# Performance work log

Measured on AMD Instinct MI355X. Metric: run time of the kernel, lower is better.

Reference implementation:

```python
import math
import jax, jax.numpy as jnp
import numpy as np
from jax import lax

B, C, H, W, D = 8, 3, 512, 512, 256
KS, SIGMA = 13, 2.0  # GaussianBlur(13); torchvision samples sigma in (0.1,5.0) -> fixed for determinism


def tanh01(v):
    return jnp.tanh(v) * 0.5 + 0.5


def tanh_range(v, left, right):
    return tanh01(v) * (right - left) + left


def norm01(v):
    return (v - v.min()) / (v.max() - v.min())


def gaussian_blur(x):
    r = KS // 2
    t = jnp.arange(KS, dtype=x.dtype) - r
    k = jnp.exp(-(t ** 2) / (2.0 * SIGMA ** 2))
    k = k / k.sum()
    b, c, h, w = x.shape
    xp = jnp.pad(x, ((0, 0), (0, 0), (r, r), (r, r)), mode='reflect').reshape(b * c, 1, h + 2 * r, w + 2 * r)
    y = lax.conv_general_dilated(xp, k.reshape(1, 1, KS, 1), (1, 1), 'VALID')
    y = lax.conv_general_dilated(y, k.reshape(1, 1, 1, KS), (1, 1), 'VALID')
    return y.reshape(b, c, h, w)


def dark_channel(x):
    return x.min(axis=1, keepdims=True)


def atmospheric_light(x, dark, top_k=1000):
    b, _, h, w = x.shape
    imsz = h * w
    numpx = max(imsz // top_k, 1)
    darkvec = dark.reshape(b, imsz)
    imvec = x.reshape(b, 3, imsz).transpose(0, 2, 1)  # [b, imsz, 3]
    idx = jnp.argsort(darkvec, axis=1)[:, imsz - numpx:]  # brightest dark-channel pixels
    gathered = jnp.take_along_axis(imvec, idx[:, :, None], axis=1)  # [b, numpx, 3]
    a = gathered[:, 1:, :].sum(axis=1) / numpx  # original loop skips index 0 of the slice
    return a[:, :, None, None]  # [b,3,1,1]


def fft_filter(x, rate, fft_gate):
    # rate: [b,1]; replicate torch.fft.fftshift default (shifts ALL axes, incl. batch/channel)
    b, c, w, h = x.shape  # note: original names w,h = shape[-2:]
    line = jnp.floor(jnp.sqrt(w * h * rate) / 2.0).astype(jnp.int32).reshape(-1)  # [b]
    rows = jnp.arange(w)
    cols = jnp.arange(h)
    mr = (rows[None, :] >= w // 2 - line[:, None]) & (rows[None, :] < w // 2 + line[:, None])
    mc = (cols[None, :] >= h // 2 - line[:, None]) & (cols[None, :] < h // 2 + line[:, None])
    mask = (mr[:, None, :, None] & mc[:, None, None, :]).astype(x.dtype)  # [b,1,w,h]
    mask = jnp.broadcast_to(mask, x.shape)
    F = jnp.fft.fftshift(jnp.fft.fft2(x, norm='forward'))
    F = F * (1.0 - mask)
    inv = jnp.fft.ifft2(jnp.fft.ifftshift(F), norm='forward').real
    return jnp.abs(inv) * fft_gate[:, None, None, None]


def setup_inputs() -> dict:
    key = jax.random.key(0)
    ks = jax.random.split(key, 20)
    def lin_w(k, i, o):
        return (jax.random.normal(k, (i, o)) * 0.02).astype(jnp.float32)
    def lin_b(k, o):
        return (jax.random.normal(k, (o,)) * 0.02).astype(jnp.float32)
    return {
        'x': jax.random.uniform(ks[0], (B, C, H, W), dtype=jnp.float32),
        'latent': (jax.random.normal(ks[1], (B, D)) * 0.5).astype(jnp.float32),
        'gate_w': lin_w(ks[2], D, 8), 'gate_b': lin_b(ks[3], 8),
        'wb_w': lin_w(ks[4], D, 3), 'wb_b': lin_b(ks[5], 3),
        'gamma_w': lin_w(ks[6], D, 1), 'gamma_b': lin_b(ks[7], 1),
        'sharp_w': lin_w(ks[8], D, 1), 'sharp_b': lin_b(ks[9], 1),
        'defog_w': lin_w(ks[10], D, 1), 'defog_b': lin_b(ks[11], 1),
        'contrast_w': lin_w(ks[12], D, 1), 'contrast_b': lin_b(ks[13], 1),
        'tone_w': lin_w(ks[14], D, 8), 'tone_b': lin_b(ks[15], 8),
        'fft_w': lin_w(ks[16], D, 1), 'fft_b': lin_b(ks[17], 1),
    }


def reference(x, latent, gate_w, gate_b, wb_w, wb_b, gamma_w, gamma_b, sharp_w, sharp_b,
              defog_w, defog_b, contrast_w, contrast_b, tone_w, tone_b, fft_w, fft_b):
    gate = tanh_range(latent @ gate_w + gate_b, 0.01, 1.0)  # [B,8]

    # white balance
    wb = jnp.exp(tanh_range(latent @ wb_w + wb_b, -0.5, 0.5))
    cs = 1.0 / (1e-5 + 0.27 * wb[:, 0] + 0.67 * wb[:, 1] + 0.06 * wb[:, 2])
    wb = cs[:, None] * wb
    wb_out = norm01(wb[:, :, None, None] * x) * gate[:, 0][:, None, None, None]

    # gamma balance
    lg = math.log(2.5)
    gamma = jnp.exp(tanh_range(latent @ gamma_w + gamma_b, -lg, lg))[:, :, None, None]
    g_out = norm01(jnp.maximum(x, 1e-4) ** gamma) * gate[:, 1][:, None, None, None]

    # identity
    id_out = x * gate[:, 2][:, None, None, None]

    # sharpening
    y = tanh_range(latent @ sharp_w + sharp_b, 0.1, 1.0)[:, :, None, None]
    s = x + y * (x - gaussian_blur(x))
    sharp_out = norm01(s) * gate[:, 3][:, None, None, None]

    # defog (atmospheric scattering model)
    omega = tanh_range(latent @ defog_w + defog_b, 0.1, 1.0)[:, :, None, None]
    dark = dark_channel(x)
    a = atmospheric_light(x, dark)
    t = 1.0 - omega * dark_channel(x / a)
    j = (x - a) / jnp.maximum(t, 0.01) + a
    fog_out = norm01(j) * gate[:, 4][:, None, None, None]

    # contrast
    alpha = jnp.tanh(latent @ contrast_w + contrast_b)[:, :, None, None]
    lum = jnp.clip(0.27 * x[:, 0] + 0.67 * x[:, 1] + 0.06 * x[:, 2], 0.0, 1.0)[:, None]
    clum = -jnp.cos(math.pi * lum) * 0.5 + 0.5
    cimg = x / (lum + 1e-6) * clum
    cimg = (1.0 - alpha) * x + alpha * cimg
    contrast_out = norm01(cimg) * gate[:, 5][:, None, None, None]

    # tone curve (8 fixed segments)
    tc = tanh_range(latent @ tone_w + tone_b, 0.5, 2.0)  # [B,8]
    tsum = tc.sum(axis=1) + 1e-30
    total = jnp.zeros_like(x)
    for i in range(8):
        total = total + jnp.clip(x - i / 8.0, 0.0, 1.0 / 8.0) * tc[:, i][:, None, None, None]
    total = total * (8.0 / tsum)[:, None, None, None]
    tone_out = norm01(total) * gate[:, 6][:, None, None, None]

    # fft frequency masking
    rate = tanh_range(latent @ fft_w + fft_b, 0.1, 0.8)  # [B,1]
    fft_out = fft_filter(x, rate, gate[:, 7])

    return norm01(wb_out + g_out + id_out + sharp_out + fog_out + contrast_out + tone_out + fft_out)
```

## Files before the change

### kernel.cpp

```cpp
#include <hip/hip_runtime.h>
#include <math.h>

#define HW 262144
#define TOTAL 6291456
#define PI_F 3.14159265358979323846f
#define NBIN 1024
#define PIDX(i) ((i) + ((i) >> 3))


#define PF_GATE 0
#define PF_WB 64
#define PF_GAMMA 88
#define PF_Y 96
#define PF_OMEGA 104
#define PF_ALPHA 112
#define PF_TC 120
#define PF_TSC 184
#define PF_RATE 192
#define PF_FG 200
#define PF_A 208
#define PF_WBM 256
#define PF_WBA 264
#define PF_GM 272
#define PF_GA 280
#define PF_SM 288
#define PF_SA 296
#define PF_FM 304
#define PF_FA 312
#define PF_CM 320
#define PF_CA 328
#define PF_TM 336
#define PF_TA 344
#define PF_LINE 360
#define PF_TCS 368
#define PF_TPRE 432
#define PF_IA 496

#define QX(b,c) ((b)*3+(c))
#define QS 24
#define QJ 25
#define QC 26
#define QFIN 27
#define SL_LCOUNT 1792
#define SL_BINSTAR 1920
#define SL_RNEED 1928
#define SL_SUMA2 2048

struct GK { float w[13]; };

__device__ __forceinline__ void waveFence(){ __builtin_amdgcn_wave_barrier(); }

__device__ __forceinline__ unsigned fkey(float f){
    unsigned u = __float_as_uint(f);
    return (u & 0x80000000u) ? ~u : (u | 0x80000000u);
}
__device__ __forceinline__ float funkey(unsigned k){
    return (k & 0x80000000u) ? __uint_as_float(k & 0x7FFFFFFFu) : __uint_as_float(~k);
}

__device__ __forceinline__ void blockRedPair(unsigned kmn, unsigned kmx, int q,
                                             unsigned* slots, unsigned* lds8){
    #pragma unroll
    for (int o = 32; o > 0; o >>= 1){
        kmn = min(kmn, __shfl_down(kmn, o));
        kmx = max(kmx, __shfl_down(kmx, o));
    }
    int w = threadIdx.x >> 6;
    if ((threadIdx.x & 63) == 0){ lds8[w] = kmn; lds8[4+w] = kmx; }
    __syncthreads();
    if (threadIdx.x == 0){
        unsigned mn = min(min(lds8[0],lds8[1]), min(lds8[2],lds8[3]));
        unsigned mx = max(max(lds8[4],lds8[5]), max(lds8[6],lds8[7]));
        int s = blockIdx.x & 31;
        atomicMin(&slots[q*64 + s], mn);
        atomicMax(&slots[q*64 + 32 + s], mx);
    }
    __syncthreads();
}

__device__ __forceinline__ float toneF(float v, const float* tc, float tsc){
    float tn = 0.f;
    #pragma unroll
    for (int i = 0; i < 8; ++i){
        float d = v - 0.125f * (float)i;
        d = fminf(fmaxf(d, 0.f), 0.125f);
        tn += d * tc[i];
    }
    return tn * tsc;
}

__device__ __forceinline__ float2 cadd(float2 a, float2 b){ return make_float2(a.x+b.x, a.y+b.y); }
__device__ __forceinline__ float2 csub(float2 a, float2 b){ return make_float2(a.x-b.x, a.y-b.y); }
__device__ __forceinline__ float2 cmul(float2 a, float2 b){ return make_float2(a.x*b.x - a.y*b.y, a.x*b.y + a.y*b.x); }

template<int S>
__device__ __forceinline__ float2 rot90(float2 z){
    return (S < 0) ? make_float2(z.y, -z.x) : make_float2(-z.y, z.x);
}

template<int S>
__device__ __forceinline__ void fft4p(float2 a, float2 b, float2 c, float2 d,
                                      float2& X0, float2& X1, float2& X2, float2& X3){
    float2 t0 = cadd(a,c), t1 = csub(a,c), t2 = cadd(b,d), t3 = csub(b,d);
    float2 it3 = rot90<S>(t3);
    X0 = cadd(t0,t2); X2 = csub(t0,t2);
    X1 = cadd(t1,it3); X3 = csub(t1,it3);
}

template<int S>
__device__ __forceinline__ void bfly8(float2 v[8]){
    const float C = 0.70710678118654752f;
    float2 E0,E1,E2,E3,O0,O1,O2,O3;
    fft4p<S>(v[0],v[2],v[4],v[6], E0,E1,E2,E3);
    fft4p<S>(v[1],v[3],v[5],v[7], O0,O1,O2,O3);
    float2 w1 = make_float2(C, (S<0) ? -C : C);
    float2 w3 = make_float2(-C, (S<0) ? -C : C);
    float2 u1 = cmul(O1, w1);
    float2 u2 = rot90<S>(O2);
    float2 u3 = cmul(O3, w3);
    v[0]=cadd(E0,O0); v[4]=csub(E0,O0);
    v[1]=cadd(E1,u1); v[5]=csub(E1,u1);
    v[2]=cadd(E2,u2); v[6]=csub(E2,u2);
    v[3]=cadd(E3,u3); v[7]=csub(E3,u3);
}

__device__ __forceinline__ void twiddles(float2 v[8], float th){
    float sn, cs; __sincosf(th, &sn, &cs);
    float2 w1 = make_float2(cs, sn);
    float2 w = w1;
    v[1] = cmul(v[1], w1);
    #pragma unroll
    for (int r = 2; r < 8; ++r){ w = cmul(w, w1); v[r] = cmul(v[r], w); }
}

template<int S>
__device__ __forceinline__ void fft512reg(float2 v[8], float2* buf, int lane){
    bfly8<S>(v);
    #pragma unroll
    for (int q = 0; q < 8; ++q) buf[PIDX(8*lane + q)] = v[q];
    waveFence();
    #pragma unroll
    for (int r = 0; r < 8; ++r) v[r] = buf[PIDX(lane + 64*r)];
    waveFence();
    twiddles(v, (float)S * 6.2831853072f * (float)(lane & 7) * (1.0f/64.0f));
    bfly8<S>(v);
    {
        int basei = ((lane >> 3) << 6) + (lane & 7);
        #pragma unroll
        for (int q = 0; q < 8; ++q) buf[PIDX(basei + 8*q)] = v[q];
    }
    waveFence();
    #pragma unroll
    for (int r = 0; r < 8; ++r) v[r] = buf[PIDX(lane + 64*r)];
    waveFence();
    twiddles(v, (float)S * 6.2831853072f * (float)lane * (1.0f/512.0f));
    bfly8<S>(v);
}

__global__ __launch_bounds__(256) void kSetup(
    const float* __restrict__ lat,
    const float* gw, const float* gb, const float* wbw, const float* wbb,
    const float* gaw, const float* gab, const float* shw, const float* shb,
    const float* dfw, const float* dfb, const float* ctw, const float* ctb,
    const float* tow, const float* tob, const float* ffw, const float* ffb,
    float* P, unsigned* slots, unsigned* hist)
{
    if (blockIdx.x != 0){
        int i = (blockIdx.x - 1) * 256 + threadIdx.x;
        if (i < 4096) slots[i] = (i < 1792 && (i & 63) < 32) ? 0xFFFFFFFFu : 0u;
        if (i < 8192) hist[i] = 0u;
        return;
    }
    int t = threadIdx.x;
    if (t < 192){
        int b = t / 24, o = t % 24;
        const float* L = lat + b * 256;
        const float* W; float bias; int nc, col;
        if (o < 8)      { W=gw;  bias=gb[o];     nc=8; col=o;    }
        else if (o < 11){ W=wbw; bias=wbb[o-8];  nc=3; col=o-8;  }
        else if (o==11) { W=gaw; bias=gab[0];    nc=1; col=0;    }
        else if (o==12) { W=shw; bias=shb[0];    nc=1; col=0;    }
        else if (o==13) { W=dfw; bias=dfb[0];    nc=1; col=0;    }
        else if (o==14) { W=ctw; bias=ctb[0];    nc=1; col=0;    }
        else if (o<23)  { W=tow; bias=tob[o-15]; nc=8; col=o-15; }
        else            { W=ffw; bias=ffb[0];    nc=1; col=0;    }
        float acc = bias;
        for (int d = 0; d < 256; ++d) acc += L[d] * W[d*nc + col];
        float t01 = tanhf(acc) * 0.5f + 0.5f;
        if (o < 8){ float v = t01*0.99f + 0.01f; P[PF_GATE + b*8 + o] = v; if (o==7) P[PF_FG + b] = v; }
        else if (o < 11){ P[PF_WB + b*3 + (o-8)] = expf(t01 - 0.5f); }
        else if (o==11){ float lg = logf(2.5f); P[PF_GAMMA + b] = expf(t01*(2.f*lg) - lg); }
        else if (o==12){ P[PF_Y + b] = t01*0.9f + 0.1f; }
        else if (o==13){ P[PF_OMEGA + b] = t01*0.9f + 0.1f; }
        else if (o==14){ P[PF_ALPHA + b] = tanhf(acc); }
        else if (o<23){ P[PF_TC + b*8 + (o-15)] = t01*1.5f + 0.5f; }
        else { P[PF_RATE + b] = t01*0.7f + 0.1f; }
    }
    __syncthreads();
    if (t < 8){
        int b = t;
        float w0=P[PF_WB+b*3], w1=P[PF_WB+b*3+1], w2=P[PF_WB+b*3+2];
        float cs = 1.0f / (1e-5f + 0.27f*w0 + 0.67f*w1 + 0.06f*w2);
        P[PF_WB+b*3] = cs*w0; P[PF_WB+b*3+1] = cs*w1; P[PF_WB+b*3+2] = cs*w2;
        float ts = 0.f;
        for (int i = 0; i < 8; ++i) ts += P[PF_TC + b*8 + i];
        float tsc = 8.0f / (ts + 1e-30f);
        P[PF_TSC + b] = tsc;
        float acc = 0.f;
        for (int k = 0; k < 8; ++k){
            float tck = P[PF_TC + b*8 + k] * tsc;
            P[PF_TCS + b*8 + k] = tck;
            P[PF_TPRE + b*8 + k] = acc;
            acc += tck * 0.125f;
        }
        int bs = (b + 4) & 7;
        ((int*)(P + PF_LINE))[b] = (int)floorf(sqrtf(262144.0f * P[PF_RATE + bs]) * 0.5f);
    }
}

__global__ __launch_bounds__(256) void kMinmaxHist(const float* __restrict__ x, unsigned* slots, unsigned* hist){
    __shared__ unsigned h[NBIN];
    __shared__ unsigned lds8[8];
    int b = blockIdx.x >> 7;
    int blk = blockIdx.x & 127;
    for (int i = threadIdx.x; i < NBIN; i += 256) h[i] = 0u;
    __syncthreads();
    size_t xb = (size_t)b*3*HW;
    int p0 = (((blk<<1)    )*256 + threadIdx.x) << 2;
    int p1 = (((blk<<1) + 1)*256 + threadIdx.x) << 2;
    float4 u0 = *(const float4*)(x + xb + p0);
    float4 u1 = *(const float4*)(x + xb + HW + p0);
    float4 u2 = *(const float4*)(x + xb + 2*HW + p0);
    float4 w0 = *(const float4*)(x + xb + p1);
    float4 w1 = *(const float4*)(x + xb + HW + p1);
    float4 w2 = *(const float4*)(x + xb + 2*HW + p1);
    float a0[8] = {u0.x,u0.y,u0.z,u0.w, w0.x,w0.y,w0.z,w0.w};
    float a1[8] = {u1.x,u1.y,u1.z,u1.w, w1.x,w1.y,w1.z,w1.w};
    float a2[8] = {u2.x,u2.y,u2.z,u2.w, w2.x,w2.y,w2.z,w2.w};
    float mn0=1e30f,mx0=-1e30f,mn1=1e30f,mx1=-1e30f,mn2=1e30f,mx2=-1e30f;
    #pragma unroll
    for (int e = 0; e < 8; ++e){
        float dark = fminf(a0[e], fminf(a1[e], a2[e]));
        atomicAdd(&h[min(NBIN-1, (int)(dark * (float)NBIN))], 1u);
        mn0 = fminf(mn0, a0[e]); mx0 = fmaxf(mx0, a0[e]);
        mn1 = fminf(mn1, a1[e]); mx1 = fmaxf(mx1, a1[e]);
        mn2 = fminf(mn2, a2[e]); mx2 = fmaxf(mx2, a2[e]);
    }
    __syncthreads();
    for (int i = threadIdx.x; i < NBIN; i += 256){
        unsigned c = h[i];
        if (c) atomicAdd(&hist[b*NBIN + i], c);
    }
    blockRedPair(fkey(mn0), fkey(mx0), QX(b,0), slots, lds8);
    blockRedPair(fkey(mn1), fkey(mx1), QX(b,1), slots, lds8);
    blockRedPair(fkey(mn2), fkey(mx2), QX(b,2), slots, lds8);
}

__global__ __launch_bounds__(256) void kScanHist(const unsigned* __restrict__ hist, unsigned* slots){
    int b = blockIdx.x, t = threadIdx.x;
    __shared__ unsigned wtot[4];
    __shared__ int doneS;
    if (t == 0) doneS = 0;
    __syncthreads();
    unsigned total = 0;
    for (int c0 = 0; c0 < NBIN; c0 += 256){
        int binIdx = NBIN-1 - (c0 + t);
        unsigned cnt = hist[b*NBIN + binIdx];
        unsigned v = cnt;
        #pragma unroll
        for (int off = 1; off < 64; off <<= 1){
            unsigned u = __shfl_up(v, off);
            if ((t & 63) >= off) v += u;
        }
        if ((t & 63) == 63) wtot[t >> 6] = v;
        __syncthreads();
        unsigned wofs = 0;
        for (int w = 0; w < (t >> 6); ++w) wofs += wtot[w];
        unsigned incl = total + wofs + v;
        unsigned excl = incl - cnt;
        if (incl >= 261u && excl < 261u){
            slots[SL_BINSTAR + b] = (unsigned)binIdx;
            slots[SL_RNEED + b]   = 261u - excl;
            doneS = 1;
        }
        __syncthreads();
        if (doneS) break;
        total += wtot[0] + wtot[1] + wtot[2] + wtot[3];
        __syncthreads();
    }
}

__global__ __launch_bounds__(256) void kCollect(const float* __restrict__ x, unsigned* slots, uint2* list){
    __shared__ float wsum[3][4];
    int b = blockIdx.x >> 8;
    int tile = blockIdx.x & 255;
    size_t xb = (size_t)b*3*HW;
    int p = (tile*256 + threadIdx.x) << 2;
    float4 v0 = *(const float4*)(x + xb + p);
    float4 v1 = *(const float4*)(x + xb + HW + p);
    float4 v2 = *(const float4*)(x + xb + 2*HW + p);
    int bs = (int)slots[SL_BINSTAR + b];
    float a0[4] = {v0.x,v0.y,v0.z,v0.w};
    float a1[4] = {v1.x,v1.y,v1.z,v1.w};
    float a2[4] = {v2.x,v2.y,v2.z,v2.w};
    float s0 = 0.f, s1 = 0.f, s2 = 0.f;
    #pragma unroll
    for (int e = 0; e < 4; ++e){
        float dark = fminf(a0[e], fminf(a1[e], a2[e]));
        int bin = min(NBIN-1, (int)(dark * (float)NBIN));
        if (bin > bs){ s0 += a0[e]; s1 += a1[e]; s2 += a2[e]; }
        else if (bin == bs){
            unsigned n = atomicAdd(&slots[SL_LCOUNT + b], 1u);
            if (n < 1024u) list[(b << 10) + n] = make_uint2(__float_as_uint(dark), (unsigned)(p + e));
        }
    }
    #pragma unroll
    for (int o = 32; o > 0; o >>= 1){
        s0 += __shfl_down(s0, o); s1 += __shfl_down(s1, o); s2 += __shfl_down(s2, o);
    }
    int w = threadIdx.x >> 6;
    if ((threadIdx.x & 63) == 0){ wsum[0][w] = s0; wsum[1][w] = s1; wsum[2][w] = s2; }
    __syncthreads();
    if (threadIdx.x == 0){
        float t0 = wsum[0][0]+wsum[0][1]+wsum[0][2]+wsum[0][3];
        float t1 = wsum[1][0]+wsum[1][1]+wsum[1][2]+wsum[1][3];
        float t2 = wsum[2][0]+wsum[2][1]+wsum[2][2]+wsum[2][3];
        float* F = (float*)(slots + SL_SUMA2);
        int sl = blockIdx.x & 31;
        atomicAdd(&F[(b*3+0)*32 + sl], t0);
        atomicAdd(&F[(b*3+1)*32 + sl], t1);
        atomicAdd(&F[(b*3+2)*32 + sl], t2);
    }
}

__global__ void kSelect(const float* __restrict__ x, uint2* list, unsigned* slots, float* P){
    __shared__ unsigned pid[262];
    __shared__ char taken[1024];
    int b = blockIdx.x, t = threadIdx.x;
    int n = (int)min(slots[SL_LCOUNT + b], 1024u);
    int r = (int)slots[SL_RNEED + b];
    if (r > n) r = n;
    const uint2* L = &list[b << 10];
    for (int i = t; i < n; i += 64) taken[i] = 0;
    __syncthreads();
    for (int it = 0; it < r; ++it){
        unsigned long long bk = 0ull; int bp = -1;
        for (int i = t; i < n; i += 64){
            if (taken[i]) continue;
            uint2 e = L[i];
            unsigned long long key = ((unsigned long long)e.x << 32) | e.y;
            if (key > bk){ bk = key; bp = i; }
        }
        #pragma unroll
        for (int o = 32; o > 0; o >>= 1){
            unsigned long long ok = __shfl_down(bk, o);
            int op = __shfl_down(bp, o);
            if (ok > bk){ bk = ok; bp = op; }
        }
        bp = __shfl(bp, 0);
        if (t == 0){ pid[it] = L[bp].y; taken[bp] = 1; }
        __syncthreads();
    }
    float s0 = 0.f, s1 = 0.f, s2 = 0.f;
    size_t xb = (size_t)b*3*HW;
    for (int i = t; i < r; i += 64){
        unsigned id = pid[i];
        s0 += x[xb + id]; s1 += x[xb + HW + id]; s2 += x[xb + 2*HW + id];
    }
    #pragma unroll
    for (int o = 32; o > 0; o >>= 1){
        s0 += __shfl_down(s0, o); s1 += __shfl_down(s1, o); s2 += __shfl_down(s2, o);
    }
    if (t == 0){
        const float* F = (const float*)(slots + SL_SUMA2);
        float f0 = 0.f, f1 = 0.f, f2 = 0.f;
        for (int k = 0; k < 32; ++k){
            f0 += F[(b*3+0)*32 + k];
            f1 += F[(b*3+1)*32 + k];
            f2 += F[(b*3+2)*32 + k];
        }
        float A0 = (s0 + f0) / 262.0f, A1 = (s1 + f1) / 262.0f, A2 = (s2 + f2) / 262.0f;
        P[PF_A + b*3+0] = A0; P[PF_A + b*3+1] = A1; P[PF_A + b*3+2] = A2;
        P[PF_IA + b*3+0] = 1.0f/A0; P[PF_IA + b*3+1] = 1.0f/A1; P[PF_IA + b*3+2] = 1.0f/A2;
    }
}

__global__ __launch_bounds__(256) void kBlur(const float* __restrict__ x, float* __restrict__ sharpOut,
                                             const float* __restrict__ P, unsigned* slots, GK gk){
    __shared__ float tile[76][80];
    __shared__ float hbuf[76][68];
    __shared__ unsigned lds8[8];
    int img = blockIdx.x >> 6;
    int tid = blockIdx.x & 63;
    int tr0 = (tid >> 3) << 6;
    int tc0 = (tid & 7) << 6;
    size_t ib = (size_t)img * HW;
    int t = threadIdx.x;
    for (int l = t; l < 76*76; l += 256){
        int r = l / 76, c = l - r*76;
        int gr = tr0 + r - 6; gr = (gr < 0) ? -gr : ((gr > 511) ? 1022 - gr : gr);
        int gc = tc0 + c - 6; gc = (gc < 0) ? -gc : ((gc > 511) ? 1022 - gc : gc);
        tile[r][c] = x[ib + ((size_t)gr << 9) + gc];
    }
    __syncthreads();
    for (int l = t; l < 76*64; l += 256){
        int r = l >> 6, c = l & 63;
        float acc = 0.f;
        #pragma unroll
        for (int k = 0; k < 13; ++k) acc += gk.w[k] * tile[r][c + k];
        hbuf[r][c] = acc;
    }
    __syncthreads();
    float yb = P[PF_Y + img/3];
    unsigned kmn = 0xFFFFFFFFu, kmx = 0u;
    for (int l = t; l < 64*64; l += 256){
        int r = l >> 6, c = l & 63;
        float acc = 0.f;
        #pragma unroll
        for (int k = 0; k < 13; ++k) acc += gk.w[k] * hbuf[r + k][c];
        float xv = tile[r + 6][c + 6];
        float s = xv + yb * (xv - acc);
        sharpOut[ib + ((size_t)(tr0 + r) << 9) + tc0 + c] = s;
        unsigned key = fkey(s);
        kmn = min(kmn, key); kmx = max(kmx, key);
    }
    blockRedPair(kmn, kmx, QS, slots, lds8);
}

__global__ __launch_bounds__(256) void kFftRowFwdJC(const float* __restrict__ x, float2* __restrict__ bc,
                                                    const float* __restrict__ P, unsigned* slots){
    __shared__ float2 buf4[4][580];
    __shared__ unsigned lds8[8];
    float (*xs)[3][512] = reinterpret_cast<float(*)[3][512]>(&buf4[0][0]);
    int b = blockIdx.x >> 8;
    int rp = blockIdx.x & 255;
    int t = threadIdx.x;
    #pragma unroll
    for (int k = 0; k < 3; ++k){
        int l = t + (k << 8);
        int seg = l >> 7;
        int idx = (l & 127) << 2;
        int ch = seg >> 1, rr = seg & 1;
        float4 z = *(const float4*)(x + (size_t)(3*b + ch)*HW + ((size_t)(2*rp + rr) << 9) + idx);
        *(float4*)&xs[rr][ch][idx] = z;
    }
    __syncthreads();
    {
        float ia0 = P[PF_IA+b*3], ia1 = P[PF_IA+b*3+1], ia2 = P[PF_IA+b*3+2];
        float a0 = P[PF_A+b*3],  a1 = P[PF_A+b*3+1],  a2 = P[PF_A+b*3+2];
        float om = P[PF_OMEGA+b], al = P[PF_ALPHA+b];
        int rr = t >> 7, c4 = (t & 127) << 2;
        float4 xv0 = *(float4*)&xs[rr][0][c4];
        float4 xv1 = *(float4*)&xs[rr][1][c4];
        float4 xv2 = *(float4*)&xs[rr][2][c4];
        float A0[4]={xv0.x,xv0.y,xv0.z,xv0.w}, A1[4]={xv1.x,xv1.y,xv1.z,xv1.w}, A2[4]={xv2.x,xv2.y,xv2.z,xv2.w};
        float jmn = 1e30f, jmx = -1e30f, cmn = 1e30f, cmx = -1e30f;
        #pragma unroll
        for (int e = 0; e < 4; ++e){
            float x0 = A0[e], x1 = A1[e], x2 = A2[e];
            float dr = fminf(x0*ia0, fminf(x1*ia1, x2*ia2));
            float T = fmaxf(1.0f - om*dr, 0.01f);
            float rT = 1.0f / T;
            float j0 = (x0-a0)*rT + a0, j1 = (x1-a1)*rT + a1, j2 = (x2-a2)*rT + a2;
            float lum = fminf(fmaxf(0.27f*x0 + 0.67f*x1 + 0.06f*x2, 0.f), 1.f);
            float clum = -__cosf(PI_F*lum)*0.5f + 0.5f;
            float alx = (1.f - al) + al * (clum / (lum + 1e-6f));
            float c0 = x0*alx, c1 = x1*alx, c2 = x2*alx;
            jmn = fminf(jmn, fminf(j0, fminf(j1, j2))); jmx = fmaxf(jmx, fmaxf(j0, fmaxf(j1, j2)));
            cmn = fminf(cmn, fminf(c0, fminf(c1, c2))); cmx = fmaxf(cmx, fmaxf(c0, fmaxf(c1, c2)));
        }
        blockRedPair(fkey(jmn), fkey(jmx), QJ, slots, lds8);
        blockRedPair(fkey(cmn), fkey(cmx), QC, slots, lds8);
    }
    int u = t >> 6, lane = t & 63;
    int frr = u >> 1, pk = u & 1;
    float2 v[8];
    #pragma unroll
    for (int r = 0; r < 8; ++r){
        int i = lane + 64*r;
        if (pk == 0) v[r] = make_float2(xs[frr][0][i] * (1.0f/512.0f), xs[frr][1][i] * (1.0f/512.0f));
        else         v[r] = make_float2(xs[frr][2][i] * (1.0f/512.0f), 0.f);
    }
    __syncthreads();
    fft512reg<-1>(v, buf4[u], lane);
    size_t ob = (size_t)(2*b + pk)*HW + ((size_t)(2*rp + frr) << 9);
    #pragma unroll
    for (int q = 0; q < 8; ++q) bc[ob + lane + 64*q] = v[q];
}

__global__ __launch_bounds__(256) void kFftColMid(float2* __restrict__ bc, const int* __restrict__ lineS){
    int img  = blockIdx.x >> 6;
    int tile = blockIdx.x & 63;
    int c0 = tile << 3;
    int line = lineS[img >> 1];
    if (c0 >= line && c0 + 8 <= 512 - line) return;
    __shared__ float2 cb[8][580];
    int t = threadIdx.x;
    size_t ibase = (size_t)img*HW + c0;
    for (int k = 0; k < 16; ++k){
        int idx = (k << 8) + t;
        int row = idx >> 3, col = idx & 7;
        float2 z = bc[ibase + ((size_t)row << 9) + col];
        cb[col][PIDX(row)] = make_float2(z.x * (1.0f/512.0f), z.y * (1.0f/512.0f));
    }
    __syncthreads();
    int lane = t & 63, u = t >> 6;
    #pragma unroll
    for (int h = 0; h < 2; ++h){
        int col = (h << 2) + u;
        int cc = c0 + col;
        bool colM = (cc < line) || (cc >= 512 - line);
        float2 v[8];
        #pragma unroll
        for (int r = 0; r < 8; ++r) v[r] = cb[col][PIDX(lane + 64*r)];
        waveFence();
        fft512reg<-1>(v, cb[col], lane);
        if (colM){
            #pragma unroll
            for (int q = 0; q < 8; ++q){
                int f = lane + (q << 6);
                if (f < line || f >= 512 - line) v[q] = make_float2(0.f, 0.f);
            }
        }
        waveFence();
        fft512reg<+1>(v, cb[col], lane);
        #pragma unroll
        for (int q = 0; q < 8; ++q) cb[col][PIDX(lane + 64*q)] = v[q];
        waveFence();
    }
    __syncthreads();
    for (int k = 0; k < 16; ++k){
        int idx = (k << 8) + t;
        int row = idx >> 3, col = idx & 7;
        int cc = c0 + col;
        if (cc < line || cc >= 512 - line)
            bc[ibase + ((size_t)row << 9) + col] = cb[col][PIDX(row)];
    }
}

__global__ __launch_bounds__(256) void kCombineFFT(const float* __restrict__ x, float* __restrict__ outb,
                                                   const float2* __restrict__ bc, const float* __restrict__ P,
                                                   unsigned* slots){
    __shared__ float2 buf4[4][580];
    __shared__ float stc[8], spre[8];
    __shared__ unsigned lds8[8];
    float (*fbuf)[3][512] = reinterpret_cast<float(*)[3][512]>(&buf4[0][0]);
    int b = blockIdx.x >> 8;
    int rp = blockIdx.x & 255;
    int t = threadIdx.x;
    if (t < 8){ stc[t] = P[PF_TCS + b*8 + t]; spre[t] = P[PF_TPRE + b*8 + t]; }
    int u = t >> 6, lane = t & 63;
    int frr = u >> 1, pk = u & 1;
    float2 v[8];
    size_t ib = (size_t)(2*b + pk)*HW + ((size_t)(2*rp + frr) << 9);
    #pragma unroll
    for (int r = 0; r < 8; ++r) v[r] = bc[ib + lane + 64*r];
    fft512reg<+1>(v, buf4[u], lane);
    __syncthreads();
    if (pk == 0){
        #pragma unroll
        for (int q = 0; q < 8; ++q){
            int i = lane + 64*q;
            fbuf[frr][0][i] = fabsf(v[q].x);
            fbuf[frr][1][i] = fabsf(v[q].y);
        }
    } else {
        #pragma unroll
        for (int q = 0; q < 8; ++q) fbuf[frr][2][lane + 64*q] = fabsf(v[q].x);
    }
    __syncthreads();

    float g  = P[PF_FG + b];
    float wb0=P[PF_WB+b*3], wb1=P[PF_WB+b*3+1], wb2=P[PF_WB+b*3+2];
    float gam=P[PF_GAMMA+b], om=P[PF_OMEGA+b], al=P[PF_ALPHA+b];
    float a0=P[PF_A+b*3], a1=P[PF_A+b*3+1], a2=P[PF_A+b*3+2];
    float ia0=P[PF_IA+b*3], ia1=P[PF_IA+b*3+1], ia2=P[PF_IA+b*3+2];
    float g2=P[PF_GATE+b*8+2];
    float wbm=P[PF_WBM+b], wba=P[PF_WBA+b], gm=P[PF_GM+b], ga=P[PF_GA+b];
    float sm=P[PF_SM+b], sa=P[PF_SA+b], fm=P[PF_FM+b], fa=P[PF_FA+b];
    float cm=P[PF_CM+b], ca=P[PF_CA+b], tm=P[PF_TM+b], ta=P[PF_TA+b];
    float kadd = wba + ga + sa + fa + ca + ta;
    float cw0 = wb0*wbm + g2, cw1 = wb1*wbm + g2, cw2 = wb2*wbm + g2;

    int rr = t >> 7, c4 = (t & 127) << 2;
    size_t p0 = (size_t)(3*b)*HW + ((size_t)(2*rp + rr) << 9) + c4;
    float4 xv0 = *(const float4*)(x + p0);
    float4 xv1 = *(const float4*)(x + p0 + HW);
    float4 xv2 = *(const float4*)(x + p0 + 2*HW);
    float4 sv0 = *(const float4*)(outb + p0);
    float4 sv1 = *(const float4*)(outb + p0 + HW);
    float4 sv2 = *(const float4*)(outb + p0 + 2*HW);
    float4 fv0 = *(float4*)&fbuf[rr][0][c4];
    float4 fv1 = *(float4*)&fbuf[rr][1][c4];
    float4 fv2 = *(float4*)&fbuf[rr][2][c4];
    float X0[4]={xv0.x,xv0.y,xv0.z,xv0.w}, X1[4]={xv1.x,xv1.y,xv1.z,xv1.w}, X2[4]={xv2.x,xv2.y,xv2.z,xv2.w};
    float S0[4]={sv0.x,sv0.y,sv0.z,sv0.w}, S1[4]={sv1.x,sv1.y,sv1.z,sv1.w}, S2[4]={sv2.x,sv2.y,sv2.z,sv2.w};
    float F0[4]={fv0.x,fv0.y,fv0.z,fv0.w}, F1[4]={fv1.x,fv1.y,fv1.z,fv1.w}, F2[4]={fv2.x,fv2.y,fv2.z,fv2.w};
    float O0[4], O1[4], O2[4];
    float mn = 1e30f, mx = -1e30f;
    #pragma unroll
    for (int e = 0; e < 4; ++e){
        float x0 = X0[e], x1 = X1[e], x2 = X2[e];
        float dr = fminf(x0*ia0, fminf(x1*ia1, x2*ia2));
        float T = fmaxf(1.0f - om*dr, 0.01f);
        float rT = 1.0f / T;
        float lum = fminf(fmaxf(0.27f*x0 + 0.67f*x1 + 0.06f*x2, 0.f), 1.f);
        float clum = -__cosf(PI_F*lum)*0.5f + 0.5f;
        float alx = (1.f - al) + al * (clum / (lum + 1e-6f));
        {
            float j = (x0 - a0)*rT + a0;
            int k = min(7, (int)(x0 * 8.0f));
            float tn = spre[k] + (x0 - 0.125f*(float)k) * stc[k];
            float gp = __powf(fmaxf(x0, 1e-4f), gam);
            float sum = x0*cw0 + gp*gm + S0[e]*sm + j*fm + (x0*alx)*cm + tn*tm + kadd + F0[e]*g;
            O0[e] = sum; mn = fminf(mn, sum); mx = fmaxf(mx, sum);
        }
        {
            float j = (x1 - a1)*rT + a1;
            int k = min(7, (int)(x1 * 8.0f));
            float tn = spre[k] + (x1 - 0.125f*(float)k) * stc[k];
            float gp = __powf(fmaxf(x1, 1e-4f), gam);
            float sum = x1*cw1 + gp*gm + S1[e]*sm + j*fm + (x1*alx)*cm + tn*tm + kadd + F1[e]*g;
            O1[e] = sum; mn = fminf(mn, sum); mx = fmaxf(mx, sum);
        }
        {
            float j = (x2 - a2)*rT + a2;
            int k = min(7, (int)(x2 * 8.0f));
            float tn = spre[k] + (x2 - 0.125f*(float)k) * stc[k];
            float gp = __powf(fmaxf(x2, 1e-4f), gam);
            float sum = x2*cw2 + gp*gm + S2[e]*sm + j*fm + (x2*alx)*cm + tn*tm + kadd + F2[e]*g;
            O2[e] = sum; mn = fminf(mn, sum); mx = fmaxf(mx, sum);
        }
    }
    *(float4*)(outb + p0)        = make_float4(O0[0],O0[1],O0[2],O0[3]);
    *(float4*)(outb + p0 + HW)   = make_float4(O1[0],O1[1],O1[2],O1[3]);
    *(float4*)(outb + p0 + 2*HW) = make_float4(O2[0],O2[1],O2[2],O2[3]);
    blockRedPair(fkey(mn), fkey(mx), QFIN, slots, lds8);
}

__global__ void kNormParams(float* P, const unsigned* __restrict__ slots){
    __shared__ float mnv[28], mxv[28];
    int t = threadIdx.x;
    if (t < 28){
        unsigned kmn = 0xFFFFFFFFu, kmx = 0u;
        for (int s = 0; s < 32; ++s){
            kmn = min(kmn, slots[t*64 + s]);
            kmx = max(kmx, slots[t*64 + 32 + s]);
        }
        mnv[t] = funkey(kmn); mxv[t] = funkey(kmx);
    }
    __syncthreads();
    if (t == 0){
        float wmin=1e30f, wmax=-1e30f, gmin=1e30f, gmax=-1e30f, tmin=1e30f, tmax=-1e30f;
        for (int b = 0; b < 8; ++b){
            float gam = P[PF_GAMMA+b];
            float tsc = P[PF_TSC+b];
            const float* tc = &P[PF_TC + b*8];
            float xbmin = 1e30f, xbmax = -1e30f;
            for (int c = 0; c < 3; ++c){
                int i = b*3 + c;
                float w = P[PF_WB + i];
                wmin = fminf(wmin, w * mnv[i]); wmax = fmaxf(wmax, w * mxv[i]);
                gmin = fminf(gmin, __powf(fmaxf(mnv[i], 1e-4f), gam));
                gmax = fmaxf(gmax, __powf(fmaxf(mxv[i], 1e-4f), gam));
                xbmin = fminf(xbmin, mnv[i]); xbmax = fmaxf(xbmax, mxv[i]);
            }
            tmin = fminf(tmin, toneF(xbmin, tc, tsc));
            tmax = fmaxf(tmax, toneF(xbmax, tc, tsc));
        }
        float smin = mnv[QS], smax = mxv[QS];
        float jmin = mnv[QJ], jmax = mxv[QJ];
        float cmin = mnv[QC], cmax = mxv[QC];
        for (int b = 0; b < 8; ++b){
            const float* G = &P[PF_GATE + b*8];
            float m;
            m = G[0]/(wmax-wmin); P[PF_WBM+b]=m; P[PF_WBA+b]=-wmin*m;
            m = G[1]/(gmax-gmin); P[PF_GM +b]=m; P[PF_GA +b]=-gmin*m;
            m = G[3]/(smax-smin); P[PF_SM +b]=m; P[PF_SA +b]=-smin*m;
            m = G[4]/(jmax-jmin); P[PF_FM +b]=m; P[PF_FA +b]=-jmin*m;
            m = G[5]/(cmax-cmin); P[PF_CM +b]=m; P[PF_CA +b]=-cmin*m;
            m = G[6]/(tmax-tmin); P[PF_TM +b]=m; P[PF_TA +b]=-tmin*m;
        }
    }
}

__global__ __launch_bounds__(256) void kFinalNorm(float* __restrict__ out, const unsigned* __restrict__ slots){
    unsigned kmn = 0xFFFFFFFFu, kmx = 0u;
    for (int s = 0; s < 32; ++s){
        kmn = min(kmn, slots[QFIN*64 + s]);
        kmx = max(kmx, slots[QFIN*64 + 32 + s]);
    }
    float mn = funkey(kmn), mx = funkey(kmx);
    float inv = 1.0f / (mx - mn);
    size_t i = ((size_t)blockIdx.x*256 + threadIdx.x) << 2;
    float4 v = *(const float4*)(out + i);
    v.x = (v.x - mn) * inv; v.y = (v.y - mn) * inv;
    v.z = (v.z - mn) * inv; v.w = (v.w - mn) * inv;
    *(float4*)(out + i) = v;
}

extern "C" void kernel_launch(void* const* d_in, const int* in_sizes, int n_in,
                              void* d_out, int out_size, void* d_ws, size_t ws_size,
                              hipStream_t stream){
    const float* x   = (const float*)d_in[0];
    const float* lat = (const float*)d_in[1];
    const float* gw  = (const float*)d_in[2];  const float* gb  = (const float*)d_in[3];
    const float* wbw = (const float*)d_in[4];  const float* wbb = (const float*)d_in[5];
    const float* gaw = (const float*)d_in[6];  const float* gab = (const float*)d_in[7];
    const float* shw = (const float*)d_in[8];  const float* shb = (const float*)d_in[9];
    const float* dfw = (const float*)d_in[10]; const float* dfb = (const float*)d_in[11];
    const float* ctw = (const float*)d_in[12]; const float* ctb = (const float*)d_in[13];
    const float* tow = (const float*)d_in[14]; const float* tob = (const float*)d_in[15];
    const float* ffw = (const float*)d_in[16]; const float* ffb = (const float*)d_in[17];
    float* out = (float*)d_out;
    char* ws = (char*)d_ws;

    float*    P     = (float*)ws;
    unsigned* slots = (unsigned*)(ws + 4096);
    unsigned* hist  = (unsigned*)(ws + 20480);
    uint2*    list  = (uint2*)(ws + 540672);
    float2*   bufC  = (float2*)(ws + 1048576);
    const int* lineS = (const int*)(P + PF_LINE);

    GK gk;
    {
        float s = 0.f;
        for (int i = 0; i < 13; ++i){ float t = (float)i - 6.f; gk.w[i] = expf(-(t*t)/8.0f); s += gk.w[i]; }
        for (int i = 0; i < 13; ++i) gk.w[i] /= s;
    }

    hipLaunchKernelGGL(kSetup,       dim3(41),   dim3(256), 0, stream, lat, gw,gb,wbw,wbb,gaw,gab,shw,shb,dfw,dfb,ctw,ctb,tow,tob,ffw,ffb, P, slots, hist);
    hipLaunchKernelGGL(kMinmaxHist,  dim3(1024), dim3(256), 0, stream, x, slots, hist);
    hipLaunchKernelGGL(kScanHist,    dim3(8),    dim3(256), 0, stream, hist, slots);
    hipLaunchKernelGGL(kCollect,     dim3(2048), dim3(256), 0, stream, x, slots, list);
    hipLaunchKernelGGL(kSelect,      dim3(8),    dim3(64),  0, stream, x, list, slots, P);
    hipLaunchKernelGGL(kBlur,        dim3(1536), dim3(256), 0, stream, x, out, P, slots, gk);
    hipLaunchKernelGGL(kFftRowFwdJC, dim3(2048), dim3(256), 0, stream, x, bufC, P, slots);
    hipLaunchKernelGGL(kFftColMid,   dim3(1024), dim3(256), 0, stream, bufC, lineS);
    hipLaunchKernelGGL(kNormParams,  dim3(1),    dim3(64),  0, stream, P, slots);
    hipLaunchKernelGGL(kCombineFFT,  dim3(2048), dim3(256), 0, stream, x, out, bufC, P, slots);
    hipLaunchKernelGGL(kFinalNorm,   dim3(6144), dim3(256), 0, stream, out, slots);
}
```

Measured before the change: 200.4 us.

## Merge independent stages into combined launches to overlap FFT, histogram and blur work

```diff
diff --git a/kernel.cpp b/kernel.cpp
--- a/kernel.cpp
+++ b/kernel.cpp
@@ -218,42 +218,76 @@
     }
 }
 
-__global__ __launch_bounds__(256) void kMinmaxHist(const float* __restrict__ x, unsigned* slots, unsigned* hist){
-    __shared__ unsigned h[NBIN];
+__global__ __launch_bounds__(256) void kHistRowFwd(const float* __restrict__ x, float2* __restrict__ bc,
+                                                   unsigned* slots, unsigned* hist){
+    __shared__ float2 buf4[4][580];
     __shared__ unsigned lds8[8];
-    int b = blockIdx.x >> 7;
-    int blk = blockIdx.x & 127;
-    for (int i = threadIdx.x; i < NBIN; i += 256) h[i] = 0u;
-    __syncthreads();
-    size_t xb = (size_t)b*3*HW;
-    int p0 = (((blk<<1)    )*256 + threadIdx.x) << 2;
-    int p1 = (((blk<<1) + 1)*256 + threadIdx.x) << 2;
-    float4 u0 = *(const float4*)(x + xb + p0);
-    float4 u1 = *(const float4*)(x + xb + HW + p0);
-    float4 u2 = *(const float4*)(x + xb + 2*HW + p0);
-    float4 w0 = *(const float4*)(x + xb + p1);
-    float4 w1 = *(const float4*)(x + xb + HW + p1);
-    float4 w2 = *(const float4*)(x + xb + 2*HW + p1);
-    float a0[8] = {u0.x,u0.y,u0.z,u0.w, w0.x,w0.y,w0.z,w0.w};
-    float a1[8] = {u1.x,u1.y,u1.z,u1.w, w1.x,w1.y,w1.z,w1.w};
-    float a2[8] = {u2.x,u2.y,u2.z,u2.w, w2.x,w2.y,w2.z,w2.w};
-    float mn0=1e30f,mx0=-1e30f,mn1=1e30f,mx1=-1e30f,mn2=1e30f,mx2=-1e30f;
-    #pragma unroll
-    for (int e = 0; e < 8; ++e){
-        float dark = fminf(a0[e], fminf(a1[e], a2[e]));
-        atomicAdd(&h[min(NBIN-1, (int)(dark * (float)NBIN))], 1u);
-        mn0 = fminf(mn0, a0[e]); mx0 = fmaxf(mx0, a0[e]);
-        mn1 = fminf(mn1, a1[e]); mx1 = fmaxf(mx1, a1[e]);
-        mn2 = fminf(mn2, a2[e]); mx2 = fmaxf(mx2, a2[e]);
-    }
-    __syncthreads();
-    for (int i = threadIdx.x; i < NBIN; i += 256){
-        unsigned c = h[i];
-        if (c) atomicAdd(&hist[b*NBIN + i], c);
-    }
-    blockRedPair(fkey(mn0), fkey(mx0), QX(b,0), slots, lds8);
-    blockRedPair(fkey(mn1), fkey(mx1), QX(b,1), slots, lds8);
-    blockRedPair(fkey(mn2), fkey(mx2), QX(b,2), slots, lds8);
+    int t = threadIdx.x;
+    if (blockIdx.x < 2048){
+        float (*xs)[3][512] = reinterpret_cast<float(*)[3][512]>(&buf4[0][0]);
+        int b = blockIdx.x >> 8;
+        int rp = blockIdx.x & 255;
+        #pragma unroll
+        for (int k = 0; k < 3; ++k){
+            int l = t + (k << 8);
+            int seg = l >> 7;
+            int idx = (l & 127) << 2;
+            int ch = seg >> 1, rr = seg & 1;
+            float4 z = *(const float4*)(x + (size_t)(3*b + ch)*HW + ((size_t)(2*rp + rr) << 9) + idx);
+            *(float4*)&xs[rr][ch][idx] = z;
+        }
+        __syncthreads();
+        int u = t >> 6, lane = t & 63;
+        int frr = u >> 1, pk = u & 1;
+        float2 v[8];
+        #pragma unroll
+        for (int r = 0; r < 8; ++r){
+            int i = lane + 64*r;
+            if (pk == 0) v[r] = make_float2(xs[frr][0][i] * (1.0f/512.0f), xs[frr][1][i] * (1.0f/512.0f));
+            else         v[r] = make_float2(xs[frr][2][i] * (1.0f/512.0f), 0.f);
+        }
+        __syncthreads();
+        fft512reg<-1>(v, buf4[u], lane);
+        size_t ob = (size_t)(2*b + pk)*HW + ((size_t)(2*rp + frr) << 9);
+        #pragma unroll
+        for (int q = 0; q < 8; ++q) bc[ob + lane + 64*q] = v[q];
+    } else {
+        unsigned* h = (unsigned*)&buf4[0][0];
+        int hb = blockIdx.x - 2048;
+        int b = hb >> 7;
+        int blk = hb & 127;
+        for (int i = t; i < NBIN; i += 256) h[i] = 0u;
+        __syncthreads();
+        size_t xb = (size_t)b*3*HW;
+        int p0 = (((blk<<1)    )*256 + t) << 2;
+        int p1 = (((blk<<1) + 1)*256 + t) << 2;
+        float4 u0 = *(const float4*)(x + xb + p0);
+        float4 u1 = *(const float4*)(x + xb + HW + p0);
+        float4 u2 = *(const float4*)(x + xb + 2*HW + p0);
+        float4 w0 = *(const float4*)(x + xb + p1);
+        float4 w1 = *(const float4*)(x + xb + HW + p1);
+        float4 w2 = *(const float4*)(x + xb + 2*HW + p1);
+        float a0[8] = {u0.x,u0.y,u0.z,u0.w, w0.x,w0.y,w0.z,w0.w};
+        float a1[8] = {u1.x,u1.y,u1.z,u1.w, w1.x,w1.y,w1.z,w1.w};
+        float a2[8] = {u2.x,u2.y,u2.z,u2.w, w2.x,w2.y,w2.z,w2.w};
+        float mn0=1e30f,mx0=-1e30f,mn1=1e30f,mx1=-1e30f,mn2=1e30f,mx2=-1e30f;
+        #pragma unroll
+        for (int e = 0; e < 8; ++e){
+            float dark = fminf(a0[e], fminf(a1[e], a2[e]));
+            atomicAdd(&h[min(NBIN-1, (int)(dark * (float)NBIN))], 1u);
+            mn0 = fminf(mn0, a0[e]); mx0 = fmaxf(mx0, a0[e]);
+            mn1 = fminf(mn1, a1[e]); mx1 = fmaxf(mx1, a1[e]);
+            mn2 = fminf(mn2, a2[e]); mx2 = fmaxf(mx2, a2[e]);
+        }
+        __syncthreads();
+        for (int i = t; i < NBIN; i += 256){
+            unsigned c = h[i];
+            if (c) atomicAdd(&hist[b*NBIN + i], c);
+        }
+        blockRedPair(fkey(mn0), fkey(mx0), QX(b,0), slots, lds8);
+        blockRedPair(fkey(mn1), fkey(mx1), QX(b,1), slots, lds8);
+        blockRedPair(fkey(mn2), fkey(mx2), QX(b,2), slots, lds8);
+    }
 }
 
 __global__ __launch_bounds__(256) void kScanHist(const unsigned* __restrict__ hist, unsigned* slots){
@@ -290,46 +324,139 @@
     }
 }
 
-__global__ __launch_bounds__(256) void kCollect(const float* __restrict__ x, unsigned* slots, uint2* list){
-    __shared__ float wsum[3][4];
-    int b = blockIdx.x >> 8;
-    int tile = blockIdx.x & 255;
-    size_t xb = (size_t)b*3*HW;
-    int p = (tile*256 + threadIdx.x) << 2;
-    float4 v0 = *(const float4*)(x + xb + p);
-    float4 v1 = *(const float4*)(x + xb + HW + p);
-    float4 v2 = *(const float4*)(x + xb + 2*HW + p);
-    int bs = (int)slots[SL_BINSTAR + b];
-    float a0[4] = {v0.x,v0.y,v0.z,v0.w};
-    float a1[4] = {v1.x,v1.y,v1.z,v1.w};
-    float a2[4] = {v2.x,v2.y,v2.z,v2.w};
-    float s0 = 0.f, s1 = 0.f, s2 = 0.f;
-    #pragma unroll
-    for (int e = 0; e < 4; ++e){
-        float dark = fminf(a0[e], fminf(a1[e], a2[e]));
-        int bin = min(NBIN-1, (int)(dark * (float)NBIN));
-        if (bin > bs){ s0 += a0[e]; s1 += a1[e]; s2 += a2[e]; }
-        else if (bin == bs){
-            unsigned n = atomicAdd(&slots[SL_LCOUNT + b], 1u);
-            if (n < 1024u) list[(b << 10) + n] = make_uint2(__float_as_uint(dark), (unsigned)(p + e));
-        }
-    }
-    #pragma unroll
-    for (int o = 32; o > 0; o >>= 1){
-        s0 += __shfl_down(s0, o); s1 += __shfl_down(s1, o); s2 += __shfl_down(s2, o);
-    }
-    int w = threadIdx.x >> 6;
-    if ((threadIdx.x & 63) == 0){ wsum[0][w] = s0; wsum[1][w] = s1; wsum[2][w] = s2; }
-    __syncthreads();
-    if (threadIdx.x == 0){
-        float t0 = wsum[0][0]+wsum[0][1]+wsum[0][2]+wsum[0][3];
-        float t1 = wsum[1][0]+wsum[1][1]+wsum[1][2]+wsum[1][3];
-        float t2 = wsum[2][0]+wsum[2][1]+wsum[2][2]+wsum[2][3];
-        float* F = (float*)(slots + SL_SUMA2);
-        int sl = blockIdx.x & 31;
-        atomicAdd(&F[(b*3+0)*32 + sl], t0);
-        atomicAdd(&F[(b*3+1)*32 + sl], t1);
-        atomicAdd(&F[(b*3+2)*32 + sl], t2);
+__global__ __launch_bounds__(256) void kCCB(const float* __restrict__ x, float2* __restrict__ bc,
+                                            const int* __restrict__ lineS, unsigned* slots, uint2* list,
+                                            const float* __restrict__ P, float* __restrict__ sharpOut, GK gk){
+    __shared__ __align__(16) char smem[45056];
+    int t = threadIdx.x;
+    if (blockIdx.x < 1024){
+        int img  = blockIdx.x >> 6;
+        int tile = blockIdx.x & 63;
+        int c0 = tile << 3;
+        int line = lineS[img >> 1];
+        if (c0 >= line && c0 + 8 <= 512 - line) return;
+        float2 (*cb)[580] = reinterpret_cast<float2(*)[580]>(smem);
+        size_t ibase = (size_t)img*HW + c0;
+        for (int k = 0; k < 16; ++k){
+            int idx = (k << 8) + t;
+            int row = idx >> 3, col = idx & 7;
+            float2 z = bc[ibase + ((size_t)row << 9) + col];
+            cb[col][PIDX(row)] = make_float2(z.x * (1.0f/512.0f), z.y * (1.0f/512.0f));
+        }
+        __syncthreads();
+        int lane = t & 63, u = t >> 6;
+        #pragma unroll
+        for (int h = 0; h < 2; ++h){
+            int col = (h << 2) + u;
+            int cc = c0 + col;
+            bool colM = (cc < line) || (cc >= 512 - line);
+            float2 v[8];
+            #pragma unroll
+            for (int r = 0; r < 8; ++r) v[r] = cb[col][PIDX(lane + 64*r)];
+            waveFence();
+            fft512reg<-1>(v, cb[col], lane);
+            if (colM){
+                #pragma unroll
+                for (int q = 0; q < 8; ++q){
+                    int f = lane + (q << 6);
+                    if (f < line || f >= 512 - line) v[q] = make_float2(0.f, 0.f);
+                }
+            }
+            waveFence();
+            fft512reg<+1>(v, cb[col], lane);
+            #pragma unroll
+            for (int q = 0; q < 8; ++q) cb[col][PIDX(lane + 64*q)] = v[q];
+            waveFence();
+        }
+        __syncthreads();
+        for (int k = 0; k < 16; ++k){
+            int idx = (k << 8) + t;
+            int row = idx >> 3, col = idx & 7;
+            int cc = c0 + col;
+            if (cc < line || cc >= 512 - line)
+                bc[ibase + ((size_t)row << 9) + col] = cb[col][PIDX(row)];
+        }
+    } else if (blockIdx.x < 3072){
+        float (*wsum)[4] = reinterpret_cast<float(*)[4]>(smem);
+        int cbk = blockIdx.x - 1024;
+        int b = cbk >> 8;
+        int tile = cbk & 255;
+        size_t xb = (size_t)b*3*HW;
+        int p = (tile*256 + t) << 2;
+        float4 v0 = *(const float4*)(x + xb + p);
+        float4 v1 = *(const float4*)(x + xb + HW + p);
+        float4 v2 = *(const float4*)(x + xb + 2*HW + p);
+        int bs = (int)slots[SL_BINSTAR + b];
+        float a0[4] = {v0.x,v0.y,v0.z,v0.w};
+        float a1[4] = {v1.x,v1.y,v1.z,v1.w};
+        float a2[4] = {v2.x,v2.y,v2.z,v2.w};
+        float s0 = 0.f, s1 = 0.f, s2 = 0.f;
+        #pragma unroll
+        for (int e = 0; e < 4; ++e){
+            float dark = fminf(a0[e], fminf(a1[e], a2[e]));
+            int bin = min(NBIN-1, (int)(dark * (float)NBIN));
+            if (bin > bs){ s0 += a0[e]; s1 += a1[e]; s2 += a2[e]; }
+            else if (bin == bs){
+                unsigned n = atomicAdd(&slots[SL_LCOUNT + b], 1u);
+                if (n < 1024u) list[(b << 10) + n] = make_uint2(__float_as_uint(dark), (unsigned)(p + e));
+            }
+        }
+        #pragma unroll
+        for (int o = 32; o > 0; o >>= 1){
+            s0 += __shfl_down(s0, o); s1 += __shfl_down(s1, o); s2 += __shfl_down(s2, o);
+        }
+        int w = t >> 6;
+        if ((t & 63) == 0){ wsum[0][w] = s0; wsum[1][w] = s1; wsum[2][w] = s2; }
+        __syncthreads();
+        if (t == 0){
+            float t0 = wsum[0][0]+wsum[0][1]+wsum[0][2]+wsum[0][3];
+            float t1 = wsum[1][0]+wsum[1][1]+wsum[1][2]+wsum[1][3];
+            float t2 = wsum[2][0]+wsum[2][1]+wsum[2][2]+wsum[2][3];
+            float* F = (float*)(slots + SL_SUMA2);
+            int sl = blockIdx.x & 31;
+            atomicAdd(&F[(b*3+0)*32 + sl], t0);
+            atomicAdd(&F[(b*3+1)*32 + sl], t1);
+            atomicAdd(&F[(b*3+2)*32 + sl], t2);
+        }
+    } else {
+        float (*tile)[80] = reinterpret_cast<float(*)[80]>(smem);
+        float (*hbuf)[68] = reinterpret_cast<float(*)[68]>(smem + 24320);
+        unsigned* lds8 = reinterpret_cast<unsigned*>(smem + 44992);
+        int bb = blockIdx.x - 3072;
+        int img = bb >> 6;
+        int tid = bb & 63;
+        int tr0 = (tid >> 3) << 6;
+        int tc0 = (tid & 7) << 6;
+        size_t ib = (size_t)img * HW;
+        for (int l = t; l < 76*76; l += 256){
+            int r = l / 76, c = l - r*76;
+            int gr = tr0 + r - 6; gr = (gr < 0) ? -gr : ((gr > 511) ? 1022 - gr : gr);
+            int gc = tc0 + c - 6; gc = (gc < 0) ? -gc : ((gc > 511) ? 1022 - gc : gc);
+            tile[r][c] = x[ib + ((size_t)gr << 9) + gc];
+        }
+        __syncthreads();
+        for (int l = t; l < 76*64; l += 256){
+            int r = l >> 6, c = l & 63;
+            float acc = 0.f;
+            #pragma unroll
+            for (int k = 0; k < 13; ++k) acc += gk.w[k] * tile[r][c + k];
+            hbuf[r][c] = acc;
+        }
+        __syncthreads();
+        float yb = P[PF_Y + img/3];
+        unsigned kmn = 0xFFFFFFFFu, kmx = 0u;
+        for (int l = t; l < 64*64; l += 256){
+            int r = l >> 6, c = l & 63;
+            float acc = 0.f;
+            #pragma unroll
+            for (int k = 0; k < 13; ++k) acc += gk.w[k] * hbuf[r + k][c];
+            float xv = tile[r + 6][c + 6];
+            float s = xv + yb * (xv - acc);
+            sharpOut[ib + ((size_t)(tr0 + r) << 9) + tc0 + c] = s;
+            unsigned key = fkey(s);
+            kmn = min(kmn, key); kmx = max(kmx, key);
+        }
+        blockRedPair(kmn, kmx, QS, slots, lds8);
     }
 }
 
@@ -385,257 +512,38 @@
     }
 }
 
-__global__ __launch_bounds__(256) void kBlur(const float* __restrict__ x, float* __restrict__ sharpOut,
-                                             const float* __restrict__ P, unsigned* slots, GK gk){
-    __shared__ float tile[76][80];
-    __shared__ float hbuf[76][68];
+__global__ __launch_bounds__(256) void kJCMinmax(const float* __restrict__ x, const float* __restrict__ P, unsigned* slots){
     __shared__ unsigned lds8[8];
-    int img = blockIdx.x >> 6;
-    int tid = blockIdx.x & 63;
-    int tr0 = (tid >> 3) << 6;
-    int tc0 = (tid & 7) << 6;
-    size_t ib = (size_t)img * HW;
-    int t = threadIdx.x;
-    for (int l = t; l < 76*76; l += 256){
-        int r = l / 76, c = l - r*76;
-        int gr = tr0 + r - 6; gr = (gr < 0) ? -gr : ((gr > 511) ? 1022 - gr : gr);
-        int gc = tc0 + c - 6; gc = (gc < 0) ? -gc : ((gc > 511) ? 1022 - gc : gc);
-        tile[r][c] = x[ib + ((size_t)gr << 9) + gc];
-    }
-    __syncthreads();
-    for (int l = t; l < 76*64; l += 256){
-        int r = l >> 6, c = l & 63;
-        float acc = 0.f;
-        #pragma unroll
-        for (int k = 0; k < 13; ++k) acc += gk.w[k] * tile[r][c + k];
-        hbuf[r][c] = acc;
-    }
-    __syncthreads();
-    float yb = P[PF_Y + img/3];
-    unsigned kmn = 0xFFFFFFFFu, kmx = 0u;
-    for (int l = t; l < 64*64; l += 256){
-        int r = l >> 6, c = l & 63;
-        float acc = 0.f;
-        #pragma unroll
-        for (int k = 0; k < 13; ++k) acc += gk.w[k] * hbuf[r + k][c];
-        float xv = tile[r + 6][c + 6];
-        float s = xv + yb * (xv - acc);
-        sharpOut[ib + ((size_t)(tr0 + r) << 9) + tc0 + c] = s;
-        unsigned key = fkey(s);
-        kmn = min(kmn, key); kmx = max(kmx, key);
-    }
-    blockRedPair(kmn, kmx, QS, slots, lds8);
-}
-
-__global__ __launch_bounds__(256) void kFftRowFwdJC(const float* __restrict__ x, float2* __restrict__ bc,
-                                                    const float* __restrict__ P, unsigned* slots){
-    __shared__ float2 buf4[4][580];
-    __shared__ unsigned lds8[8];
-    float (*xs)[3][512] = reinterpret_cast<float(*)[3][512]>(&buf4[0][0]);
     int b = blockIdx.x >> 8;
-    int rp = blockIdx.x & 255;
-    int t = threadIdx.x;
-    #pragma unroll
-    for (int k = 0; k < 3; ++k){
-        int l = t + (k << 8);
-        int seg = l >> 7;
-        int idx = (l & 127) << 2;
-        int ch = seg >> 1, rr = seg & 1;
-        float4 z = *(const float4*)(x + (size_t)(3*b + ch)*HW + ((size_t)(2*rp + rr) << 9) + idx);
-        *(float4*)&xs[rr][ch][idx] = z;
-    }
-    __syncthreads();
-    {
-        float ia0 = P[PF_IA+b*3], ia1 = P[PF_IA+b*3+1], ia2 = P[PF_IA+b*3+2];
-        float a0 = P[PF_A+b*3],  a1 = P[PF_A+b*3+1],  a2 = P[PF_A+b*3+2];
-        float om = P[PF_OMEGA+b], al = P[PF_ALPHA+b];
-        int rr = t >> 7, c4 = (t & 127) << 2;
-        float4 xv0 = *(float4*)&xs[rr][0][c4];
-        float4 xv1 = *(float4*)&xs[rr][1][c4];
-        float4 xv2 = *(float4*)&xs[rr][2][c4];
-        float A0[4]={xv0.x,xv0.y,xv0.z,xv0.w}, A1[4]={xv1.x,xv1.y,xv1.z,xv1.w}, A2[4]={xv2.x,xv2.y,xv2.z,xv2.w};
-        float jmn = 1e30f, jmx = -1e30f, cmn = 1e30f, cmx = -1e30f;
-        #pragma unroll
-        for (int e = 0; e < 4; ++e){
-            float x0 = A0[e], x1 = A1[e], x2 = A2[e];
-            float dr = fminf(x0*ia0, fminf(x1*ia1, x2*ia2));
-            float T = fmaxf(1.0f - om*dr, 0.01f);
-            float rT = 1.0f / T;
-            float j0 = (x0-a0)*rT + a0, j1 = (x1-a1)*rT + a1, j2 = (x2-a2)*rT + a2;
-            float lum = fminf(fmaxf(0.27f*x0 + 0.67f*x1 + 0.06f*x2, 0.f), 1.f);
-            float clum = -__cosf(PI_F*lum)*0.5f + 0.5f;
-            float alx = (1.f - al) + al * (clum / (lum + 1e-6f));
-            float c0 = x0*alx, c1 = x1*alx, c2 = x2*alx;
-            jmn = fminf(jmn, fminf(j0, fminf(j1, j2))); jmx = fmaxf(jmx, fmaxf(j0, fmaxf(j1, j2)));
-            cmn = fminf(cmn, fminf(c0, fminf(c1, c2))); cmx = fmaxf(cmx, fmaxf(c0, fmaxf(c1, c2)));
-        }
-        blockRedPair(fkey(jmn), fkey(jmx), QJ, slots, lds8);
-        blockRedPair(fkey(cmn), fkey(cmx), QC, slots, lds8);
-    }
-    int u = t >> 6, lane = t & 63;
-    int frr = u >> 1, pk = u & 1;
-    float2 v[8];
-    #pragma unroll
-    for (int r = 0; r < 8; ++r){
-        int i = lane + 64*r;
-        if (pk == 0) v[r] = make_float2(xs[frr][0][i] * (1.0f/512.0f), xs[frr][1][i] * (1.0f/512.0f));
-        else         v[r] = make_float2(xs[frr][2][i] * (1.0f/512.0f), 0.f);
-    }
-    __syncthreads();
-    fft512reg<-1>(v, buf4[u], lane);
-    size_t ob = (size_t)(2*b + pk)*HW + ((size_t)(2*rp + frr) << 9);
-    #pragma unroll
-    for (int q = 0; q < 8; ++q) bc[ob + lane + 64*q] = v[q];
-}
-
-__global__ __launch_bounds__(256) void kFftColMid(float2* __restrict__ bc, const int* __restrict__ lineS){
-    int img  = blockIdx.x >> 6;
-    int tile = blockIdx.x & 63;
-    int c0 = tile << 3;
-    int line = lineS[img >> 1];
-    if (c0 >= line && c0 + 8 <= 512 - line) return;
-    __shared__ float2 cb[8][580];
-    int t = threadIdx.x;
-    size_t ibase = (size_t)img*HW + c0;
-    for (int k = 0; k < 16; ++k){
-        int idx = (k << 8) + t;
-        int row = idx >> 3, col = idx & 7;
-        float2 z = bc[ibase + ((size_t)row << 9) + col];
-        cb[col][PIDX(row)] = make_float2(z.x * (1.0f/512.0f), z.y * (1.0f/512.0f));
-    }
-    __syncthreads();
-    int lane = t & 63, u = t >> 6;
-    #pragma unroll
-    for (int h = 0; h < 2; ++h){
-        int col = (h << 2) + u;
-        int cc = c0 + col;
-        bool colM = (cc < line) || (cc >= 512 - line);
-        float2 v[8];
-        #pragma unroll
-        for (int r = 0; r < 8; ++r) v[r] = cb[col][PIDX(lane + 64*r)];
-        waveFence();
-        fft512reg<-1>(v, cb[col], lane);
-        if (colM){
-            #pragma unroll
-            for (int q = 0; q < 8; ++q){
-                int f = lane + (q << 6);
-                if (f < line || f >= 512 - line) v[q] = make_float2(0.f, 0.f);
-            }
-        }
-        waveFence();
-        fft512reg<+1>(v, cb[col], lane);
-        #pragma unroll
-        for (int q = 0; q < 8; ++q) cb[col][PIDX(lane + 64*q)] = v[q];
-        waveFence();
-    }
-    __syncthreads();
-    for (int k = 0; k < 16; ++k){
-        int idx = (k << 8) + t;
-        int row = idx >> 3, col = idx & 7;
-        int cc = c0 + col;
-        if (cc < line || cc >= 512 - line)
-            bc[ibase + ((size_t)row << 9) + col] = cb[col][PIDX(row)];
-    }
-}
-
-__global__ __launch_bounds__(256) void kCombineFFT(const float* __restrict__ x, float* __restrict__ outb,
-                                                   const float2* __restrict__ bc, const float* __restrict__ P,
-                                                   unsigned* slots){
-    __shared__ float2 buf4[4][580];
-    __shared__ float stc[8], spre[8];
-    __shared__ unsigned lds8[8];
-    float (*fbuf)[3][512] = reinterpret_cast<float(*)[3][512]>(&buf4[0][0]);
-    int b = blockIdx.x >> 8;
-    int rp = blockIdx.x & 255;
-    int t = threadIdx.x;
-    if (t < 8){ stc[t] = P[PF_TCS + b*8 + t]; spre[t] = P[PF_TPRE + b*8 + t]; }
-    int u = t >> 6, lane = t & 63;
-    int frr = u >> 1, pk = u & 1;
-    float2 v[8];
-    size_t ib = (size_t)(2*b + pk)*HW + ((size_t)(2*rp + frr) << 9);
-    #pragma unroll
-    for (int r = 0; r < 8; ++r) v[r] = bc[ib + lane + 64*r];
-    fft512reg<+1>(v, buf4[u], lane);
-    __syncthreads();
-    if (pk == 0){
-        #pragma unroll
-        for (int q = 0; q < 8; ++q){
-            int i = lane + 64*q;
-            fbuf[frr][0][i] = fabsf(v[q].x);
-            fbuf[frr][1][i] = fabsf(v[q].y);
-        }
-    } else {
-        #pragma unroll
-        for (int q = 0; q < 8; ++q) fbuf[frr][2][lane + 64*q] = fabsf(v[q].x);
-    }
-    __syncthreads();
-
-    float g  = P[PF_FG + b];
-    float wb0=P[PF_WB+b*3], wb1=P[PF_WB+b*3+1], wb2=P[PF_WB+b*3+2];
-    float gam=P[PF_GAMMA+b], om=P[PF_OMEGA+b], al=P[PF_ALPHA+b];
-    float a0=P[PF_A+b*3], a1=P[PF_A+b*3+1], a2=P[PF_A+b*3+2];
-    float ia0=P[PF_IA+b*3], ia1=P[PF_IA+b*3+1], ia2=P[PF_IA+b*3+2];
-    float g2=P[PF_GATE+b*8+2];
-    float wbm=P[PF_WBM+b], wba=P[PF_WBA+b], gm=P[PF_GM+b], ga=P[PF_GA+b];
-    float sm=P[PF_SM+b], sa=P[PF_SA+b], fm=P[PF_FM+b], fa=P[PF_FA+b];
-    float cm=P[PF_CM+b], ca=P[PF_CA+b], tm=P[PF_TM+b], ta=P[PF_TA+b];
-    float kadd = wba + ga + sa + fa + ca + ta;
-    float cw0 = wb0*wbm + g2, cw1 = wb1*wbm + g2, cw2 = wb2*wbm + g2;
-
-    int rr = t >> 7, c4 = (t & 127) << 2;
-    size_t p0 = (size_t)(3*b)*HW + ((size_t)(2*rp + rr) << 9) + c4;
-    float4 xv0 = *(const float4*)(x + p0);
-    float4 xv1 = *(const float4*)(x + p0 + HW);
-    float4 xv2 = *(const float4*)(x + p0 + 2*HW);
-    float4 sv0 = *(const float4*)(outb + p0);
-    float4 sv1 = *(const float4*)(outb + p0 + HW);
-    float4 sv2 = *(const float4*)(outb + p0 + 2*HW);
-    float4 fv0 = *(float4*)&fbuf[rr][0][c4];
-    float4 fv1 = *(float4*)&fbuf[rr][1][c4];
-    float4 fv2 = *(float4*)&fbuf[rr][2][c4];
-    float X0[4]={xv0.x,xv0.y,xv0.z,xv0.w}, X1[4]={xv1.x,xv1.y,xv1.z,xv1.w}, X2[4]={xv2.x,xv2.y,xv2.z,xv2.w};
-    float S0[4]={sv0.x,sv0.y,sv0.z,sv0.w}, S1[4]={sv1.x,sv1.y,sv1.z,sv1.w}, S2[4]={sv2.x,sv2.y,sv2.z,sv2.w};
-    float F0[4]={fv0.x,fv0.y,fv0.z,fv0.w}, F1[4]={fv1.x,fv1.y,fv1.z,fv1.w}, F2[4]={fv2.x,fv2.y,fv2.z,fv2.w};
-    float O0[4], O1[4], O2[4];
-    float mn = 1e30f, mx = -1e30f;
+    int tile = blockIdx.x & 255;
+    size_t xb = (size_t)b*3*HW;
+    int p = (tile*256 + threadIdx.x) << 2;
+    float4 v0 = *(const float4*)(x + xb + p);
+    float4 v1 = *(const float4*)(x + xb + HW + p);
+    float4 v2 = *(const float4*)(x + xb + 2*HW + p);
+    float ia0 = P[PF_IA+b*3], ia1 = P[PF_IA+b*3+1], ia2 = P[PF_IA+b*3+2];
+    float a0 = P[PF_A+b*3],  a1 = P[PF_A+b*3+1],  a2 = P[PF_A+b*3+2];
+    float om = P[PF_OMEGA+b], al = P[PF_ALPHA+b];
+    float a0v[4] = {v0.x,v0.y,v0.z,v0.w};
+    float a1v[4] = {v1.x,v1.y,v1.z,v1.w};
+    float a2v[4] = {v2.x,v2.y,v2.z,v2.w};
+    float jmn = 1e30f, jmx = -1e30f, cmn = 1e30f, cmx = -1e30f;
     #pragma unroll
     for (int e = 0; e < 4; ++e){
-        float x0 = X0[e], x1 = X1[e], x2 = X2[e];
+        float x0 = a0v[e], x1 = a1v[e], x2 = a2v[e];
         float dr = fminf(x0*ia0, fminf(x1*ia1, x2*ia2));
         float T = fmaxf(1.0f - om*dr, 0.01f);
         float rT = 1.0f / T;
+        float j0 = (x0-a0)*rT + a0, j1 = (x1-a1)*rT + a1, j2 = (x2-a2)*rT + a2;
         float lum = fminf(fmaxf(0.27f*x0 + 0.67f*x1 + 0.06f*x2, 0.f), 1.f);
         float clum = -__cosf(PI_F*lum)*0.5f + 0.5f;
         float alx = (1.f - al) + al * (clum / (lum + 1e-6f));
-        {
-            float j = (x0 - a0)*rT + a0;
-            int k = min(7, (int)(x0 * 8.0f));
-            float tn = spre[k] + (x0 - 0.125f*(float)k) * stc[k];
-            float gp = __powf(fmaxf(x0, 1e-4f), gam);
-            float sum = x0*cw0 + gp*gm + S0[e]*sm + j*fm + (x0*alx)*cm + tn*tm + kadd + F0[e]*g;
-            O0[e] = sum; mn = fminf(mn, sum); mx = fmaxf(mx, sum);
-        }
-        {
-            float j = (x1 - a1)*rT + a1;
-            int k = min(7, (int)(x1 * 8.0f));
-            float tn = spre[k] + (x1 - 0.125f*(float)k) * stc[k];
-            float gp = __powf(fmaxf(x1, 1e-4f), gam);
-            float sum = x1*cw1 + gp*gm + S1[e]*sm + j*fm + (x1*alx)*cm + tn*tm + kadd + F1[e]*g;
-            O1[e] = sum; mn = fminf(mn, sum); mx = fmaxf(mx, sum);
-        }
-        {
-            float j = (x2 - a2)*rT + a2;
-            int k = min(7, (int)(x2 * 8.0f));
-            float tn = spre[k] + (x2 - 0.125f*(float)k) * stc[k];
-            float gp = __powf(fmaxf(x2, 1e-4f), gam);
-            float sum = x2*cw2 + gp*gm + S2[e]*sm + j*fm + (x2*alx)*cm + tn*tm + kadd + F2[e]*g;
-            O2[e] = sum; mn = fminf(mn, sum); mx = fmaxf(mx, sum);
-        }
-    }
-    *(float4*)(outb + p0)        = make_float4(O0[0],O0[1],O0[2],O0[3]);
-    *(float4*)(outb + p0 + HW)   = make_float4(O1[0],O1[1],O1[2],O1[3]);
-    *(float4*)(outb + p0 + 2*HW) = make_float4(O2[0],O2[1],O2[2],O2[3]);
-    blockRedPair(fkey(mn), fkey(mx), QFIN, slots, lds8);
+        float c0 = x0*alx, c1 = x1*alx, c2 = x2*alx;
+        jmn = fminf(jmn, fminf(j0, fminf(j1, j2))); jmx = fmaxf(jmx, fmaxf(j0, fmaxf(j1, j2)));
+        cmn = fminf(cmn, fminf(c0, fminf(c1, c2))); cmx = fmaxf(cmx, fmaxf(c0, fmaxf(c1, c2)));
+    }
+    blockRedPair(fkey(jmn), fkey(jmx), QJ, slots, lds8);
+    blockRedPair(fkey(cmn), fkey(cmx), QC, slots, lds8);
 }
 
 __global__ void kNormParams(float* P, const unsigned* __restrict__ slots){
@@ -684,6 +592,106 @@
     }
 }
 
+__global__ __launch_bounds__(256) void kCombineFFT(const float* __restrict__ x, float* __restrict__ outb,
+                                                   const float2* __restrict__ bc, const float* __restrict__ P,
+                                                   unsigned* slots){
+    __shared__ float2 buf4[4][580];
+    __shared__ float stc[8], spre[8];
+    __shared__ unsigned lds8[8];
+    float (*fbuf)[3][512] = reinterpret_cast<float(*)[3][512]>(&buf4[0][0]);
+    int b = blockIdx.x >> 8;
+    int rp = blockIdx.x & 255;
+    int t = threadIdx.x;
+    if (t < 8){ stc[t] = P[PF_TCS + b*8 + t]; spre[t] = P[PF_TPRE + b*8 + t]; }
+    int u = t >> 6, lane = t & 63;
+    int frr = u >> 1, pk = u & 1;
+    float2 v[8];
+    size_t ib = (size_t)(2*b + pk)*HW + ((size_t)(2*rp + frr) << 9);
+    #pragma unroll
+    for (int r = 0; r < 8; ++r) v[r] = bc[ib + lane + 64*r];
+    fft512reg<+1>(v, buf4[u], lane);
+    __syncthreads();
+    if (pk == 0){
+        #pragma unroll
+        for (int q = 0; q < 8; ++q){
+            int i = lane + 64*q;
+            fbuf[frr][0][i] = fabsf(v[q].x);
+            fbuf[frr][1][i] = fabsf(v[q].y);
+        }
+    } else {
+        #pragma unroll
+        for (int q = 0; q < 8; ++q) fbuf[frr][2][lane + 64*q] = fabsf(v[q].x);
+    }
+    __syncthreads();
+
+    float g  = P[PF_FG + b];
+    float wb0=P[PF_WB+b*3], wb1=P[PF_WB+b*3+1], wb2=P[PF_WB+b*3+2];
+    float gam=P[PF_GAMMA+b], om=P[PF_OMEGA+b], al=P[PF_ALPHA+b];
+    float a0=P[PF_A+b*3], a1=P[PF_A+b*3+1], a2=P[PF_A+b*3+2];
+    float ia0=P[PF_IA+b*3], ia1=P[PF_IA+b*3+1], ia2=P[PF_IA+b*3+2];
+    float g2=P[PF_GATE+b*8+2];
+    float wbm=P[PF_WBM+b], wba=P[PF_WBA+b], gm=P[PF_GM+b], ga=P[PF_GA+b];
+    float sm=P[PF_SM+b], sa=P[PF_SA+b], fm=P[PF_FM+b], fa=P[PF_FA+b];
+    float cm=P[PF_CM+b], ca=P[PF_CA+b], tm=P[PF_TM+b], ta=P[PF_TA+b];
+    float kadd = wba + ga + sa + fa + ca + ta;
+    float cw0 = wb0*wbm + g2, cw1 = wb1*wbm + g2, cw2 = wb2*wbm + g2;
+
+    int rr = t >> 7, c4 = (t & 127) << 2;
+    size_t p0 = (size_t)(3*b)*HW + ((size_t)(2*rp + rr) << 9) + c4;
+    float4 xv0 = *(const float4*)(x + p0);
+    float4 xv1 = *(const float4*)(x + p0 + HW);
+    float4 xv2 = *(const float4*)(x + p0 + 2*HW);
+    float4 sv0 = *(const float4*)(outb + p0);
+    float4 sv1 = *(const float4*)(outb + p0 + HW);
+    float4 sv2 = *(const float4*)(outb + p0 + 2*HW);
+    float4 fv0 = *(float4*)&fbuf[rr][0][c4];
+    float4 fv1 = *(float4*)&fbuf[rr][1][c4];
+    float4 fv2 = *(float4*)&fbuf[rr][2][c4];
+    float X0[4]={xv0.x,xv0.y,xv0.z,xv0.w}, X1[4]={xv1.x,xv1.y,xv1.z,xv1.w}, X2[4]={xv2.x,xv2.y,xv2.z,xv2.w};
+    float S0[4]={sv0.x,sv0.y,sv0.z,sv0.w}, S1[4]={sv1.x,sv1.y,sv1.z,sv1.w}, S2[4]={sv2.x,sv2.y,sv2.z,sv2.w};
+    float F0[4]={fv0.x,fv0.y,fv0.z,fv0.w}, F1[4]={fv1.x,fv1.y,fv1.z,fv1.w}, F2[4]={fv2.x,fv2.y,fv2.z,fv2.w};
+    float O0[4], O1[4], O2[4];
+    float mn = 1e30f, mx = -1e30f;
+    #pragma unroll
+    for (int e = 0; e < 4; ++e){
+        float x0 = X0[e], x1 = X1[e], x2 = X2[e];
+        float dr = fminf(x0*ia0, fminf(x1*ia1, x2*ia2));
+        float T = fmaxf(1.0f - om*dr, 0.01f);
+        float rT = 1.0f / T;
+        float lum = fminf(fmaxf(0.27f*x0 + 0.67f*x1 + 0.06f*x2, 0.f), 1.f);
+        float clum = -__cosf(PI_F*lum)*0.5f + 0.5f;
+        float alx = (1.f - al) + al * (clum / (lum + 1e-6f));
+        {
+            float j = (x0 - a0)*rT + a0;
+            int k = min(7, (int)(x0 * 8.0f));
+            float tn = spre[k] + (x0 - 0.125f*(float)k) * stc[k];
+            float gp = __powf(fmaxf(x0, 1e-4f), gam);
+            float sum = x0*cw0 + gp*gm + S0[e]*sm + j*fm + (x0*alx)*cm + tn*tm + kadd + F0[e]*g;
+            O0[e] = sum; mn = fminf(mn, sum); mx = fmaxf(mx, sum);
+        }
+        {
+            float j = (x1 - a1)*rT + a1;
+            int k = min(7, (int)(x1 * 8.0f));
+            float tn = spre[k] + (x1 - 0.125f*(float)k) * stc[k];
+            float gp = __powf(fmaxf(x1, 1e-4f), gam);
+            float sum = x1*cw1 + gp*gm + S1[e]*sm + j*fm + (x1*alx)*cm + tn*tm + kadd + F1[e]*g;
+            O1[e] = sum; mn = fminf(mn, sum); mx = fmaxf(mx, sum);
+        }
+        {
+            float j = (x2 - a2)*rT + a2;
+            int k = min(7, (int)(x2 * 8.0f));
+            float tn = spre[k] + (x2 - 0.125f*(float)k) * stc[k];
+            float gp = __powf(fmaxf(x2, 1e-4f), gam);
+            float sum = x2*cw2 + gp*gm + S2[e]*sm + j*fm + (x2*alx)*cm + tn*tm + kadd + F2[e]*g;
+            O2[e] = sum; mn = fminf(mn, sum); mx = fmaxf(mx, sum);
+        }
+    }
+    *(float4*)(outb + p0)        = make_float4(O0[0],O0[1],O0[2],O0[3]);
+    *(float4*)(outb + p0 + HW)   = make_float4(O1[0],O1[1],O1[2],O1[3]);
+    *(float4*)(outb + p0 + 2*HW) = make_float4(O2[0],O2[1],O2[2],O2[3]);
+    blockRedPair(fkey(mn), fkey(mx), QFIN, slots, lds8);
+}
+
 __global__ __launch_bounds__(256) void kFinalNorm(float* __restrict__ out, const unsigned* __restrict__ slots){
     unsigned kmn = 0xFFFFFFFFu, kmx = 0u;
     for (int s = 0; s < 32; ++s){
@@ -730,13 +738,11 @@
     }
 
     hipLaunchKernelGGL(kSetup,       dim3(41),   dim3(256), 0, stream, lat, gw,gb,wbw,wbb,gaw,gab,shw,shb,dfw,dfb,ctw,ctb,tow,tob,ffw,ffb, P, slots, hist);
-    hipLaunchKernelGGL(kMinmaxHist,  dim3(1024), dim3(256), 0, stream, x, slots, hist);
+    hipLaunchKernelGGL(kHistRowFwd,  dim3(3072), dim3(256), 0, stream, x, bufC, slots, hist);
     hipLaunchKernelGGL(kScanHist,    dim3(8),    dim3(256), 0, stream, hist, slots);
-    hipLaunchKernelGGL(kCollect,     dim3(2048), dim3(256), 0, stream, x, slots, list);
+    hipLaunchKernelGGL(kCCB,         dim3(4608), dim3(256), 0, stream, x, bufC, lineS, slots, list, P, out, gk);
     hipLaunchKernelGGL(kSelect,      dim3(8),    dim3(64),  0, stream, x, list, slots, P);
-    hipLaunchKernelGGL(kBlur,        dim3(1536), dim3(256), 0, stream, x, out, P, slots, gk);
-    hipLaunchKernelGGL(kFftRowFwdJC, dim3(2048), dim3(256), 0, stream, x, bufC, P, slots);
-    hipLaunchKernelGGL(kFftColMid,   dim3(1024), dim3(256), 0, stream, bufC, lineS);
+    hipLaunchKernelGGL(kJCMinmax,    dim3(2048), dim3(256), 0, stream, x, P, slots);
     hipLaunchKernelGGL(kNormParams,  dim3(1),    dim3(64),  0, stream, P, slots);
     hipLaunchKernelGGL(kCombineFFT,  dim3(2048), dim3(256), 0, stream, x, out, bufC, P, slots);
     hipLaunchKernelGGL(kFinalNorm,   dim3(6144), dim3(256), 0, stream, out, slots);
```

New measurement: 198.9 us. Within noise of the previous version (-0.8%).
